# Kernel optimization log

Hardware: AMD Instinct MI355X
Metric: run time of the kernel (lower is better)

Reference implementation:

```python
import jax, jax.numpy as jnp
import numpy as np

B = 32768   # batch
F = 32      # per-node feature dim
H = 256     # hidden width
M = 4       # modules per node
OUT = 8     # final output dim
INIT_W = 0.003
B_INIT = 0.1


def _lin(k, din, dout):
    # fanin_init-style uniform weights, bias filled with 0.1 (hidden layers)
    s = 1.0 / np.sqrt(din)
    W = jax.random.uniform(k, (M, din, dout), jnp.float32, -s, s)
    b = jnp.full((M, dout), B_INIT, jnp.float32)
    return W, b


def setup_inputs() -> dict:
    key = jax.random.key(0)
    ks = jax.random.split(key, 16)
    feats = jax.random.normal(ks[0], (B, 4 * F), jnp.float32)
    idx = jax.random.randint(ks[1], (B, 4), 0, M)
    onehots = jax.nn.one_hot(idx, M, dtype=jnp.float32).reshape(B, 4 * M)
    input_val = jnp.concatenate([feats, onehots], axis=1)  # [B,144]

    W00, b00 = _lin(ks[2], F, H)        # node0 post layer 0
    W01, b01 = _lin(ks[3], H, H)        # node0 post layer 1
    Wpre1, bpre1 = _lin(ks[4], F, H)    # node1 pre
    Wpost1, bpost1 = _lin(ks[5], 2 * H, H)  # node1 interface (prev 256 + own 256)
    Wpre2, bpre2 = _lin(ks[6], F, H)
    Wpost2, bpost2 = _lin(ks[7], 2 * H, H)
    Wpre3, bpre3 = _lin(ks[8], F, H)
    Wpost3, bpost3 = _lin(ks[9], 2 * H, H)
    # final output layer: uniform(-init_w, init_w) for W and b, identity act
    Wfin3 = jax.random.uniform(ks[10], (M, H, OUT), jnp.float32, -INIT_W, INIT_W)
    bfin3 = jax.random.uniform(ks[11], (M, OUT), jnp.float32, -INIT_W, INIT_W)
    return dict(input_val=input_val,
                W00=W00, b00=b00, W01=W01, b01=b01,
                Wpre1=Wpre1, bpre1=bpre1, Wpost1=Wpost1, bpost1=bpost1,
                Wpre2=Wpre2, bpre2=bpre2, Wpost2=Wpost2, bpost2=bpost2,
                Wpre3=Wpre3, bpre3=bpre3, Wpost3=Wpost3, bpost3=bpost3,
                Wfin3=Wfin3, bfin3=bfin3)


def _select(h, onehot):
    # per-row pick of the assigned module's output: [B,M,D],[B,M] -> [B,D]
    return jnp.einsum('bmo,bm->bo', h, onehot)


def reference(input_val, W00, b00, W01, b01,
              Wpre1, bpre1, Wpost1, bpost1,
              Wpre2, bpre2, Wpost2, bpost2,
              Wpre3, bpre3, Wpost3, bpost3,
              Wfin3, bfin3):
    feat = lambda j: input_val[:, j * F:(j + 1) * F]
    oh = lambda j: input_val[:, 4 * F + j * M: 4 * F + (j + 1) * M]

    # node 0: two hidden layers, module-dispatched (dense-all-modules + one-hot combine)
    h = jax.nn.relu(jnp.einsum('bi,mio->bmo', feat(0), W00) + b00)
    h = jax.nn.relu(jnp.einsum('bmi,mio->bmo', h, W01) + b01)
    x = _select(h, oh(0))  # [B,H]

    def node(x_prev, fj, ohj, Wpre, bpre, Wpost, bpost):
        hp = jax.nn.relu(jnp.einsum('bi,mio->bmo', fj, Wpre) + bpre)
        # interface layer consumes concat([x_prev, hp]); split the weight to
        # avoid materializing [B,M,2H]
        hq = jax.nn.relu(jnp.einsum('bi,mio->bmo', x_prev, Wpost[:, :H, :])
                         + jnp.einsum('bmi,mio->bmo', hp, Wpost[:, H:, :])
                         + bpost)
        return hq  # [B,M,H]

    x = _select(node(x, feat(1), oh(1), Wpre1, bpre1, Wpost1, bpost1), oh(1))
    x = _select(node(x, feat(2), oh(2), Wpre2, bpre2, Wpost2, bpost2), oh(2))

    h3 = node(x, feat(3), oh(3), Wpre3, bpre3, Wpost3, bpost3)  # [B,M,H]
    out = jnp.einsum('bmi,mio->bmo', h3, Wfin3) + bfin3          # final linear, identity act
    return _select(out, oh(3))  # [B,OUT]
```

## Files before the change

kernel.cpp:

```cpp
#include <hip/hip_runtime.h>

#define NB 32768
#define MAXTILE 768

typedef short s8v __attribute__((ext_vector_type(8)));
typedef float f4v __attribute__((ext_vector_type(4)));
typedef unsigned short u16;
typedef unsigned int u32;
typedef unsigned char u8;

__device__ __forceinline__ float bf2f(u16 u) { return __uint_as_float(((u32)u) << 16); }
__device__ __forceinline__ u16 f2bf(float f) {
    u32 x = __float_as_uint(f);
    x += 0x7FFFu + ((x >> 16) & 1u);
    return (u16)(x >> 16);
}
__device__ __forceinline__ s8v ld8(const u16* p) { return *reinterpret_cast<const s8v*>(p); }

#define MFMA16(a, b, c) __builtin_amdgcn_mfma_f32_16x16x32_bf16((a), (b), (c), 0, 0, 0)

__global__ void probe_kernel(const void* __restrict__ input, int* __restrict__ flagp)
{
    int lane = threadIdx.x;
    u32 w = ((const u32*)input)[lane];
    u32 h0 = w & 0xFFFFu;
    u32 e0 = (h0 >> 7) & 0xFFu;
    bool plaus = (h0 == 0u) || (e0 >= 96u && e0 <= 143u);
    unsigned long long m = __ballot(plaus);
    if (lane == 0) *flagp = (__popcll(m) >= 48) ? 1 : 0;
}

struct Ent { const void* src; u16* dst; int Ksrc; int kBase; int S; };
struct RepackArgs { Ent d[11]; };
struct BEnt { const void* src; int dstOff; int n; };
struct BiasArgs { BEnt d[10]; };

__global__ __launch_bounds__(256) void prepA_kernel(const void* __restrict__ inputv,
                                                    const int* __restrict__ flagp,
                                                    int* __restrict__ counters,
                                                    u8* __restrict__ keys,
                                                    u16* __restrict__ inB,
                                                    u16* __restrict__ cbias,
                                                    RepackArgs A, BiasArgs BA)
{
    int flag = *flagp;
    if (blockIdx.x < 128) {
        __shared__ int lcnt[256];
        int tid = threadIdx.x;
        lcnt[tid] = 0;
        __syncthreads();
        int row = (blockIdx.x << 8) + tid;
        const u32* in32 = (const u32*)inputv;
        const u16* in16 = (const u16*)inputv;
        int key = 0;
#pragma unroll
        for (int j = 0; j < 4; j++) {
            int base = row * 144 + 128 + j * 4;
            u32 v1, v2, v3;
            if (flag) { v1 = in16[base + 1]; v2 = in16[base + 2]; v3 = in16[base + 3]; }
            else      { v1 = in32[base + 1]; v2 = in32[base + 2]; v3 = in32[base + 3]; }
            int m = v1 ? 1 : (v2 ? 2 : (v3 ? 3 : 0));
            key |= m << (j << 1);
        }
        keys[row] = (u8)key;
        atomicAdd(&lcnt[key], 1);
        __syncthreads();
        if (lcnt[tid]) atomicAdd(&counters[tid], lcnt[tid]);
    } else {
        const int RTOT = 131072 + 7 * 262144;
        const int BTOT = 8 * 1024 + 8192 + 32;
        const int PHA = RTOT + BTOT;
        int gtid = (blockIdx.x - 128) * 256 + threadIdx.x;
        int gstr = (gridDim.x - 128) * 256;
        int TOT = flag ? PHA : PHA + NB * 144;
        for (int i = gtid; i < TOT; i += gstr) {
            if (i < RTOT) {
                int e, local;
                if (i < 131072) { e = i >> 15; local = i & 32767; }
                else { int t = i - 131072; e = 4 + (t >> 18); local = t & 262143; }
                Ent d = A.d[e];
                int jj = local & 7, lane = (local >> 3) & 63, ct = (local >> 9) & 15;
                int m, s;
                if (d.S == 1) { m = local >> 13; s = 0; }
                else          { m = local >> 16; s = (local >> 13) & 7; }
                int k = d.kBase + s * 32 + ((lane >> 4) << 3) + jj;
                int n = (ct << 4) + (lane & 15);
                int idx = (m * d.Ksrc + k) * 256 + n;
                d.dst[local] = flag ? ((const u16*)d.src)[idx]
                                    : f2bf(((const float*)d.src)[idx]);
            } else if (i < PHA) {
                int t = i - RTOT;
                for (int e = 0; e < 10; e++) {
                    BEnt b = BA.d[e];
                    if (t < b.n) {
                        cbias[b.dstOff + t] = flag ? ((const u16*)b.src)[t]
                                                   : f2bf(((const float*)b.src)[t]);
                        break;
                    }
                    t -= b.n;
                }
            } else {
                int t = i - PHA;
                inB[t] = f2bf(((const float*)inputv)[t]);
            }
        }
    }
}

__global__ __launch_bounds__(256) void scan_kernel(const int* __restrict__ counters,
                                                   int* __restrict__ cursors,
                                                   int4* __restrict__ tileInfo)
{
    __shared__ int sbuf[256];
    __shared__ int tot;
    int tid = threadIdx.x;
    int c = counters[tid];
    sbuf[tid] = c;
    __syncthreads();
    for (int off = 1; off < 256; off <<= 1) {
        int v = (tid >= off) ? sbuf[tid - off] : 0;
        __syncthreads();
        sbuf[tid] += v;
        __syncthreads();
    }
    int base = sbuf[tid] - c;
    cursors[tid] = base;
    int tiles = (c + 63) >> 6;
    __syncthreads();
    sbuf[tid] = tiles;
    __syncthreads();
    for (int off = 1; off < 256; off <<= 1) {
        int v = (tid >= off) ? sbuf[tid - off] : 0;
        __syncthreads();
        sbuf[tid] += v;
        __syncthreads();
    }
    int tbase = sbuf[tid] - tiles;
    if (tid == 255) tot = sbuf[255];
    __syncthreads();
    for (int t = 0; t < tiles; t++) {
        int rem = c - t * 64;
        tileInfo[tbase + t] = make_int4(tid, base + t * 64, rem > 64 ? 64 : rem, 0);
    }
    for (int i = tot + tid; i < MAXTILE; i += 256)
        tileInfo[i] = make_int4(0, 0, 0, 0);
}

__global__ __launch_bounds__(256) void prepB_kernel(const u8* __restrict__ keys,
                                                    int* __restrict__ cursors,
                                                    int* __restrict__ perm)
{
    __shared__ int lcnt[256];
    __shared__ int lbase[256];
    int tid = threadIdx.x;
    lcnt[tid] = 0;
    __syncthreads();
    int row = (blockIdx.x << 8) + tid;
    int key = keys[row];
    int loc = atomicAdd(&lcnt[key], 1);
    __syncthreads();
    if (lcnt[tid]) lbase[tid] = atomicAdd(&cursors[tid], lcnt[tid]);
    __syncthreads();
    perm[lbase[key] + loc] = row;
}

struct MainW {
    const u16* pre[4];
    const u16* A[4];
    const u16* B[4];
    int bpre[4];
    int bmain[4];
};

__global__ __launch_bounds__(512, 4) void main_kernel(
    const void* __restrict__ inRaw, const u16* __restrict__ inB,
    const int* __restrict__ flagp,
    const int* __restrict__ perm, const int4* __restrict__ tileInfo,
    const u16* __restrict__ cbias, MainW W, void* __restrict__ outp)
{
    __shared__ __align__(16) u16 xc[64 * 264];
    __shared__ __align__(16) u16 hp[64 * 264];
    __shared__ __align__(16) u16 wfl[8 * 264];
    __shared__ int rowids[64];

    int tid = threadIdx.x;
    int lane = tid & 63, wave = tid >> 6, quad = lane >> 4, l16 = lane & 15;

    int4 ti = tileInfo[blockIdx.x];
    int key = ti.x, ppos = ti.y, cntIn = ti.z;
    if (cntIn <= 0) return;
    int flag = *flagp;
    const u16* ip = flag ? (const u16*)inRaw : inB;

    if (tid < 64) {
        int g = tid < cntIn ? tid : cntIn - 1;
        rowids[tid] = perm[ppos + g];
    }
    {
        int m3 = (key >> 6) & 3;
        const u16* Wf = cbias + 8192;
        for (int i = tid; i < 2048; i += 512) {
            int k = i & 255, o = i >> 8;
            wfl[o * 264 + k] = Wf[(((m3 << 8) + k) << 3) + o];
        }
    }
    __syncthreads();

    int ct0 = wave << 1;

    for (int node = 0; node < 4; node++) {
        int m = (key >> (node << 1)) & 3;

        {
            const s8v* Bp = (const s8v*)W.pre[node] + (m << 4) * 64 + lane;
            const u16* bb = cbias + W.bpre[node] + (m << 8);
#pragma unroll
            for (int rt = 0; rt < 4; rt++) {
                int row = rowids[(rt << 4) + l16];
                s8v a = ld8(ip + row * 144 + (node << 5) + (quad << 3));
#pragma unroll
                for (int ci = 0; ci < 2; ci++) {
                    int ct = ct0 + ci;
                    f4v c = {0.f, 0.f, 0.f, 0.f};
                    c = MFMA16(a, Bp[ct * 64], c);
                    float bv = bf2f(bb[(ct << 4) + l16]);
#pragma unroll
                    for (int r = 0; r < 4; r++) {
                        float v = c[r] + bv; v = v > 0.f ? v : 0.f;
                        hp[((rt << 4) + (quad << 2) + r) * 264 + (ct << 4) + l16] = f2bf(v);
                    }
                }
            }
        }
        __syncthreads();

        f4v acc[4][2];
#pragma unroll
        for (int i = 0; i < 4; i++) { acc[i][0] = (f4v){0,0,0,0}; acc[i][1] = (f4v){0,0,0,0}; }

        if (node > 0) {
            const s8v* BA = (const s8v*)W.A[node];
#pragma unroll
            for (int s = 0; s < 8; s++) {
                s8v a0 = ld8(&xc[(l16) * 264 + (s << 5) + (quad << 3)]);
                s8v a1 = ld8(&xc[(16 + l16) * 264 + (s << 5) + (quad << 3)]);
                s8v a2 = ld8(&xc[(32 + l16) * 264 + (s << 5) + (quad << 3)]);
                s8v a3 = ld8(&xc[(48 + l16) * 264 + (s << 5) + (quad << 3)]);
#pragma unroll
                for (int ci = 0; ci < 2; ci++) {
                    s8v bv = BA[((((m << 3) + s) << 4) + ct0 + ci) * 64 + lane];
                    acc[0][ci] = MFMA16(a0, bv, acc[0][ci]);
                    acc[1][ci] = MFMA16(a1, bv, acc[1][ci]);
                    acc[2][ci] = MFMA16(a2, bv, acc[2][ci]);
                    acc[3][ci] = MFMA16(a3, bv, acc[3][ci]);
                }
            }
        }
        {
            const s8v* BB = (const s8v*)W.B[node];
#pragma unroll
            for (int s = 0; s < 8; s++) {
                s8v a0 = ld8(&hp[(l16) * 264 + (s << 5) + (quad << 3)]);
                s8v a1 = ld8(&hp[(16 + l16) * 264 + (s << 5) + (quad << 3)]);
                s8v a2 = ld8(&hp[(32 + l16) * 264 + (s << 5) + (quad << 3)]);
                s8v a3 = ld8(&hp[(48 + l16) * 264 + (s << 5) + (quad << 3)]);
#pragma unroll
                for (int ci = 0; ci < 2; ci++) {
                    s8v bv = BB[((((m << 3) + s) << 4) + ct0 + ci) * 64 + lane];
                    acc[0][ci] = MFMA16(a0, bv, acc[0][ci]);
                    acc[1][ci] = MFMA16(a1, bv, acc[1][ci]);
                    acc[2][ci] = MFMA16(a2, bv, acc[2][ci]);
                    acc[3][ci] = MFMA16(a3, bv, acc[3][ci]);
                }
            }
        }
        __syncthreads();

        {
            const u16* bm = cbias + W.bmain[node] + (m << 8);
#pragma unroll
            for (int ci = 0; ci < 2; ci++) {
                int colb = ((ct0 + ci) << 4) + l16;
                float bv = bf2f(bm[colb]);
#pragma unroll
                for (int rt = 0; rt < 4; rt++) {
#pragma unroll
                    for (int r = 0; r < 4; r++) {
                        float v = acc[rt][ci][r] + bv; v = v > 0.f ? v : 0.f;
                        xc[((rt << 4) + (quad << 2) + r) * 264 + colb] = f2bf(v);
                    }
                }
            }
        }
        __syncthreads();
    }

    {
        int m3 = (key >> 6) & 3;
        int r = tid >> 3, o = tid & 7;
        float s = bf2f(cbias[16384 + (m3 << 3) + o]);
        const u16* hrow = &xc[r * 264];
        const u16* wrow = &wfl[o * 264];
        for (int k = 0; k < 256; k += 8) {
            s8v h8 = ld8(hrow + k);
            s8v w8 = ld8(wrow + k);
#pragma unroll
            for (int j = 0; j < 8; j++) s += bf2f((u16)h8[j]) * bf2f((u16)w8[j]);
        }
        if (r < cntIn) {
            int oi = (rowids[r] << 3) + o;
            if (flag) ((u16*)outp)[oi] = f2bf(s);
            else      ((float*)outp)[oi] = s;
        }
    }
}

extern "C" void kernel_launch(void* const* d_in, const int* in_sizes, int n_in,
                              void* d_out, int out_size, void* d_ws, size_t ws_size,
                              hipStream_t stream)
{
    (void)in_sizes; (void)n_in; (void)out_size;
    const void* input  = d_in[0];
    const void* W00    = d_in[1];
    const void* b00    = d_in[2];
    const void* W01    = d_in[3];
    const void* b01    = d_in[4];
    const void* Wpre1  = d_in[5];
    const void* bpre1  = d_in[6];
    const void* Wpost1 = d_in[7];
    const void* bpost1 = d_in[8];
    const void* Wpre2  = d_in[9];
    const void* bpre2  = d_in[10];
    const void* Wpost2 = d_in[11];
    const void* bpost2 = d_in[12];
    const void* Wpre3  = d_in[13];
    const void* bpre3  = d_in[14];
    const void* Wpost3 = d_in[15];
    const void* bpost3 = d_in[16];
    const void* Wfin   = d_in[17];
    const void* bfin   = d_in[18];

    char* base = (char*)d_ws;
    size_t off = 0;
    auto alloc = [&](size_t bytes) -> char* {
        char* p = base + off;
        off += (bytes + 255) & ~(size_t)255;
        return p;
    };
    int*  flagp    = (int*)alloc(4);
    int*  counters = (int*)alloc(256 * 4);
    int*  cursors  = (int*)alloc(256 * 4);
    u8*   keys     = (u8*)alloc(NB);
    int4* tileInfo = (int4*)alloc(MAXTILE * 16);
    int*  perm     = (int*)alloc((size_t)NB * 4);
    u16*  cbias    = (u16*)alloc(16640 * 2);
    u16*  inB      = (u16*)alloc((size_t)NB * 144 * 2);
    u16* rW00   = (u16*)alloc(32768 * 2);
    u16* rWpre1 = (u16*)alloc(32768 * 2);
    u16* rWpre2 = (u16*)alloc(32768 * 2);
    u16* rWpre3 = (u16*)alloc(32768 * 2);
    u16* rW01 = (u16*)alloc(262144 * 2);
    u16* rW1A = (u16*)alloc(262144 * 2);
    u16* rW1B = (u16*)alloc(262144 * 2);
    u16* rW2A = (u16*)alloc(262144 * 2);
    u16* rW2B = (u16*)alloc(262144 * 2);
    u16* rW3A = (u16*)alloc(262144 * 2);
    u16* rW3B = (u16*)alloc(262144 * 2);
    if (off > ws_size) return;

    hipMemsetAsync(counters, 0, 256 * 4, stream);
    probe_kernel<<<1, 64, 0, stream>>>(input, flagp);

    RepackArgs ra;
    ra.d[0]  = Ent{W00,    rW00,   32,   0, 1};
    ra.d[1]  = Ent{Wpre1,  rWpre1, 32,   0, 1};
    ra.d[2]  = Ent{Wpre2,  rWpre2, 32,   0, 1};
    ra.d[3]  = Ent{Wpre3,  rWpre3, 32,   0, 1};
    ra.d[4]  = Ent{W01,    rW01,  256,   0, 8};
    ra.d[5]  = Ent{Wpost1, rW1A,  512,   0, 8};
    ra.d[6]  = Ent{Wpost1, rW1B,  512, 256, 8};
    ra.d[7]  = Ent{Wpost2, rW2A,  512,   0, 8};
    ra.d[8]  = Ent{Wpost2, rW2B,  512, 256, 8};
    ra.d[9]  = Ent{Wpost3, rW3A,  512,   0, 8};
    ra.d[10] = Ent{Wpost3, rW3B,  512, 256, 8};

    BiasArgs ba;
    ba.d[0] = BEnt{b00,    0,     1024};
    ba.d[1] = BEnt{b01,    1024,  1024};
    ba.d[2] = BEnt{bpre1,  2048,  1024};
    ba.d[3] = BEnt{bpost1, 3072,  1024};
    ba.d[4] = BEnt{bpre2,  4096,  1024};
    ba.d[5] = BEnt{bpost2, 5120,  1024};
    ba.d[6] = BEnt{bpre3,  6144,  1024};
    ba.d[7] = BEnt{bpost3, 7168,  1024};
    ba.d[8] = BEnt{Wfin,   8192,  8192};
    ba.d[9] = BEnt{bfin,   16384, 32};

    prepA_kernel<<<128 + 1536, 256, 0, stream>>>(input, flagp, counters, keys, inB, cbias, ra, ba);
    scan_kernel<<<1, 256, 0, stream>>>(counters, cursors, tileInfo);
    prepB_kernel<<<128, 256, 0, stream>>>(keys, cursors, perm);

    MainW W;
    W.pre[0] = rW00;   W.pre[1] = rWpre1; W.pre[2] = rWpre2; W.pre[3] = rWpre3;
    W.A[0]   = nullptr; W.A[1]  = rW1A;   W.A[2]   = rW2A;   W.A[3]   = rW3A;
    W.B[0]   = rW01;   W.B[1]   = rW1B;   W.B[2]   = rW2B;   W.B[3]   = rW3B;
    W.bpre[0] = 0;    W.bpre[1] = 2048; W.bpre[2] = 4096; W.bpre[3] = 6144;
    W.bmain[0] = 1024; W.bmain[1] = 3072; W.bmain[2] = 5120; W.bmain[3] = 7168;

    main_kernel<<<MAXTILE, 512, 0, stream>>>(input, inB, flagp, perm, tileInfo, cbias, W, d_out);
}
```

Measured before the change: 203.7 us.

## Restructure main kernel with transposed MFMA, fused concat buffer, and tiled weight repack

The main kernel now computes the transposed product (weights as the A operand, activations as B) and keeps the previous node output and the pre-layer output side by side in one LDS buffer. The interface layer therefore runs as a single K=512 loop, with a register prefetch of the next weight slice and bias folded into the accumulator init. The full-input bf16 conversion pass is dropped: fp32 inputs are converted on the fly inside the main kernel. Weight repacking moves to a separate kernel that transposes through LDS per tile, the final layer uses MFMA instead of a scalar dot product, and the counter memset is folded into the probe kernel. The goal is less preprocessing traffic and fewer launches, at the cost of more complex indexing and larger LDS rows.

```diff
diff --git a/kernel.cpp b/kernel.cpp
--- a/kernel.cpp
+++ b/kernel.cpp
@@ -2,10 +2,13 @@
 
 #define NB 32768
 #define MAXTILE 768
+#define XHS 536
 
 typedef short s8v __attribute__((ext_vector_type(8)));
+typedef short s4v __attribute__((ext_vector_type(4)));
 typedef float f4v __attribute__((ext_vector_type(4)));
 typedef unsigned short u16;
+typedef unsigned short u16x4 __attribute__((ext_vector_type(4)));
 typedef unsigned int u32;
 typedef unsigned char u8;
 
@@ -19,92 +22,49 @@
 
 #define MFMA16(a, b, c) __builtin_amdgcn_mfma_f32_16x16x32_bf16((a), (b), (c), 0, 0, 0)
 
-__global__ void probe_kernel(const void* __restrict__ input, int* __restrict__ flagp)
-{
-    int lane = threadIdx.x;
-    u32 w = ((const u32*)input)[lane];
-    u32 h0 = w & 0xFFFFu;
-    u32 e0 = (h0 >> 7) & 0xFFu;
-    bool plaus = (h0 == 0u) || (e0 >= 96u && e0 <= 143u);
-    unsigned long long m = __ballot(plaus);
-    if (lane == 0) *flagp = (__popcll(m) >= 48) ? 1 : 0;
-}
-
-struct Ent { const void* src; u16* dst; int Ksrc; int kBase; int S; };
-struct RepackArgs { Ent d[11]; };
-struct BEnt { const void* src; int dstOff; int n; };
-struct BiasArgs { BEnt d[10]; };
+__global__ __launch_bounds__(256) void probe_kernel(const void* __restrict__ input,
+                                                    int* __restrict__ flagp,
+                                                    int* __restrict__ counters)
+{
+    int tid = threadIdx.x;
+    counters[tid] = 0;
+    if (tid < 64) {
+        u32 w = ((const u32*)input)[tid];
+        u32 h0 = w & 0xFFFFu;
+        u32 e0 = (h0 >> 7) & 0xFFu;
+        bool plaus = (h0 == 0u) || (e0 >= 96u && e0 <= 143u);
+        unsigned long long m = __ballot(plaus);
+        if (tid == 0) *flagp = (__popcll(m) >= 48) ? 1 : 0;
+    }
+}
 
 __global__ __launch_bounds__(256) void prepA_kernel(const void* __restrict__ inputv,
                                                     const int* __restrict__ flagp,
                                                     int* __restrict__ counters,
-                                                    u8* __restrict__ keys,
-                                                    u16* __restrict__ inB,
-                                                    u16* __restrict__ cbias,
-                                                    RepackArgs A, BiasArgs BA)
-{
+                                                    u8* __restrict__ keys)
+{
+    __shared__ int lcnt[256];
     int flag = *flagp;
-    if (blockIdx.x < 128) {
-        __shared__ int lcnt[256];
-        int tid = threadIdx.x;
-        lcnt[tid] = 0;
-        __syncthreads();
-        int row = (blockIdx.x << 8) + tid;
-        const u32* in32 = (const u32*)inputv;
-        const u16* in16 = (const u16*)inputv;
-        int key = 0;
-#pragma unroll
-        for (int j = 0; j < 4; j++) {
-            int base = row * 144 + 128 + j * 4;
-            u32 v1, v2, v3;
-            if (flag) { v1 = in16[base + 1]; v2 = in16[base + 2]; v3 = in16[base + 3]; }
-            else      { v1 = in32[base + 1]; v2 = in32[base + 2]; v3 = in32[base + 3]; }
-            int m = v1 ? 1 : (v2 ? 2 : (v3 ? 3 : 0));
-            key |= m << (j << 1);
-        }
-        keys[row] = (u8)key;
-        atomicAdd(&lcnt[key], 1);
-        __syncthreads();
-        if (lcnt[tid]) atomicAdd(&counters[tid], lcnt[tid]);
-    } else {
-        const int RTOT = 131072 + 7 * 262144;
-        const int BTOT = 8 * 1024 + 8192 + 32;
-        const int PHA = RTOT + BTOT;
-        int gtid = (blockIdx.x - 128) * 256 + threadIdx.x;
-        int gstr = (gridDim.x - 128) * 256;
-        int TOT = flag ? PHA : PHA + NB * 144;
-        for (int i = gtid; i < TOT; i += gstr) {
-            if (i < RTOT) {
-                int e, local;
-                if (i < 131072) { e = i >> 15; local = i & 32767; }
-                else { int t = i - 131072; e = 4 + (t >> 18); local = t & 262143; }
-                Ent d = A.d[e];
-                int jj = local & 7, lane = (local >> 3) & 63, ct = (local >> 9) & 15;
-                int m, s;
-                if (d.S == 1) { m = local >> 13; s = 0; }
-                else          { m = local >> 16; s = (local >> 13) & 7; }
-                int k = d.kBase + s * 32 + ((lane >> 4) << 3) + jj;
-                int n = (ct << 4) + (lane & 15);
-                int idx = (m * d.Ksrc + k) * 256 + n;
-                d.dst[local] = flag ? ((const u16*)d.src)[idx]
-                                    : f2bf(((const float*)d.src)[idx]);
-            } else if (i < PHA) {
-                int t = i - RTOT;
-                for (int e = 0; e < 10; e++) {
-                    BEnt b = BA.d[e];
-                    if (t < b.n) {
-                        cbias[b.dstOff + t] = flag ? ((const u16*)b.src)[t]
-                                                   : f2bf(((const float*)b.src)[t]);
-                        break;
-                    }
-                    t -= b.n;
-                }
-            } else {
-                int t = i - PHA;
-                inB[t] = f2bf(((const float*)inputv)[t]);
-            }
-        }
-    }
+    int tid = threadIdx.x;
+    lcnt[tid] = 0;
+    __syncthreads();
+    int row = (blockIdx.x << 8) + tid;
+    const u32* in32 = (const u32*)inputv;
+    const u16* in16 = (const u16*)inputv;
+    int key = 0;
+#pragma unroll
+    for (int j = 0; j < 4; j++) {
+        int base = row * 144 + 128 + j * 4;
+        u32 v1, v2, v3;
+        if (flag) { v1 = in16[base + 1]; v2 = in16[base + 2]; v3 = in16[base + 3]; }
+        else      { v1 = in32[base + 1]; v2 = in32[base + 2]; v3 = in32[base + 3]; }
+        int m = v1 ? 1 : (v2 ? 2 : (v3 ? 3 : 0));
+        key |= m << (j << 1);
+    }
+    keys[row] = (u8)key;
+    atomicAdd(&lcnt[key], 1);
+    __syncthreads();
+    if (lcnt[tid]) atomicAdd(&counters[tid], lcnt[tid]);
 }
 
 __global__ __launch_bounds__(256) void scan_kernel(const int* __restrict__ counters,
@@ -164,153 +124,217 @@
     perm[lbase[key] + loc] = row;
 }
 
-struct MainW {
-    const u16* pre[4];
-    const u16* A[4];
-    const u16* B[4];
-    int bpre[4];
-    int bmain[4];
+struct RepArgs {
+    const void* W01; const void* Wp[3]; const void* pre[4]; const void* fin;
+    const void* bias[9];
+    u16 *rPre, *rW01, *rWp[3], *rFin, *cbias;
 };
 
+__global__ __launch_bounds__(256) void repack_kernel(const int* __restrict__ flagp, RepArgs R)
+{
+    __shared__ u16 T[8192];
+    int flag = *flagp;
+    int tid = threadIdx.x;
+    int b = blockIdx.x;
+
+    const void* src = nullptr; u16* dst = nullptr; int K = 0, k0 = 0, mrow = 0;
+    if (b < 32) {
+        int m = b >> 3, s = b & 7;
+        src = R.W01; dst = R.rW01 + (m * 8 + s) * 8192; K = 256; k0 = s * 32; mrow = m;
+    } else if (b < 224) {
+        int idx = b - 32, mat = idx >> 6, r = idx & 63, m = r >> 4, s = r & 15;
+        src = R.Wp[mat]; dst = R.rWp[mat] + (m * 16 + s) * 8192; K = 512; k0 = s * 32; mrow = m;
+    } else if (b < 240) {
+        int idx = b - 224, mat = idx >> 2, m = idx & 3;
+        src = R.pre[mat]; dst = R.rPre + (mat * 4 + m) * 8192; K = 32; k0 = 0; mrow = m;
+    } else if (b < 244) {
+        int m = b - 240;
+        const u16* s16 = (const u16*)R.fin;
+        const float* s32 = (const float*)R.fin;
+        for (int i = tid; i < 2048; i += 256) {
+            int si = (m * 256 + (i >> 3)) * 8 + (i & 7);
+            T[i] = flag ? s16[si] : f2bf(s32[si]);
+        }
+        __syncthreads();
+        u16* d = R.rFin + m * 4096;
+        for (int i = tid; i < 4096; i += 256) {
+            int s = i >> 9, lane = (i >> 3) & 63, j = i & 7;
+            int q = lane >> 4, l16 = lane & 15;
+            int k = s * 32 + q * 8 + j;
+            d[i] = (l16 < 8) ? T[k * 8 + l16] : (u16)0;
+        }
+        return;
+    } else {
+        const int sz[9] = {1024,1024,1024,1024,1024,1024,1024,1024,32};
+        const int of[9] = {0,1024,2048,3072,4096,5120,6144,7168,8192};
+        for (int i = tid; i < 8224; i += 256) {
+            int t = i, e = 0;
+            while (t >= sz[e]) { t -= sz[e]; e++; }
+            R.cbias[of[e] + t] = flag ? ((const u16*)R.bias[e])[t]
+                                      : f2bf(((const float*)R.bias[e])[t]);
+        }
+        return;
+    }
+
+    const u16* s16 = (const u16*)src;
+    const float* s32 = (const float*)src;
+    for (int i = tid; i < 8192; i += 256) {
+        int k = i >> 8, n = i & 255;
+        int srcIdx = (mrow * K + k0 + k) * 256 + n;
+        T[i] = flag ? s16[srcIdx] : f2bf(s32[srcIdx]);
+    }
+    __syncthreads();
+    for (int i = tid; i < 8192; i += 256) {
+        int mt = i >> 9, lane = (i >> 3) & 63, j = i & 7;
+        int k = ((lane >> 4) << 3) + j, n = (mt << 4) + (lane & 15);
+        dst[i] = T[(k << 8) + n];
+    }
+}
+
+struct MainP { const u16 *rPre, *rW01, *rWp1, *rWp2, *rWp3, *rFin, *cbias; };
+
 __global__ __launch_bounds__(512, 4) void main_kernel(
-    const void* __restrict__ inRaw, const u16* __restrict__ inB,
-    const int* __restrict__ flagp,
+    const void* __restrict__ inRaw, const int* __restrict__ flagp,
     const int* __restrict__ perm, const int4* __restrict__ tileInfo,
-    const u16* __restrict__ cbias, MainW W, void* __restrict__ outp)
-{
-    __shared__ __align__(16) u16 xc[64 * 264];
-    __shared__ __align__(16) u16 hp[64 * 264];
-    __shared__ __align__(16) u16 wfl[8 * 264];
+    MainP P, void* __restrict__ outp)
+{
+    __shared__ __align__(16) u16 xh[64 * XHS];
     __shared__ int rowids[64];
 
     int tid = threadIdx.x;
-    int lane = tid & 63, wave = tid >> 6, quad = lane >> 4, l16 = lane & 15;
+    int lane = tid & 63, w = tid >> 6, quad = lane >> 4, l16 = lane & 15;
 
     int4 ti = tileInfo[blockIdx.x];
     int key = ti.x, ppos = ti.y, cntIn = ti.z;
     if (cntIn <= 0) return;
     int flag = *flagp;
-    const u16* ip = flag ? (const u16*)inRaw : inB;
 
     if (tid < 64) {
         int g = tid < cntIn ? tid : cntIn - 1;
         rowids[tid] = perm[ppos + g];
     }
-    {
-        int m3 = (key >> 6) & 3;
-        const u16* Wf = cbias + 8192;
-        for (int i = tid; i < 2048; i += 512) {
-            int k = i & 255, o = i >> 8;
-            wfl[o * 264 + k] = Wf[(((m3 << 8) + k) << 3) + o];
-        }
-    }
-    __syncthreads();
-
-    int ct0 = wave << 1;
+    __syncthreads();
+    int rows[4];
+#pragma unroll
+    for (int nt = 0; nt < 4; nt++) rows[nt] = rowids[nt * 16 + l16];
+
+    const u16* mainW[4] = {P.rW01, P.rWp1, P.rWp2, P.rWp3};
+    const u16* in16 = (const u16*)inRaw;
+    const float* in32 = (const float*)inRaw;
 
     for (int node = 0; node < 4; node++) {
         int m = (key >> (node << 1)) & 3;
 
+        s8v fb[4];
+#pragma unroll
+        for (int nt = 0; nt < 4; nt++) {
+            int off = rows[nt] * 144 + (node << 5) + (quad << 3);
+            if (flag) fb[nt] = ld8(in16 + off);
+            else {
+                f4v f0 = *(const f4v*)(in32 + off);
+                f4v f1 = *(const f4v*)(in32 + off + 4);
+                s8v r;
+#pragma unroll
+                for (int j = 0; j < 4; j++) { r[j] = (short)f2bf(f0[j]); r[4 + j] = (short)f2bf(f1[j]); }
+                fb[nt] = r;
+            }
+        }
+
+        const u16* preB = P.rPre + ((node << 2) + m) * 8192;
+#pragma unroll
+        for (int ci = 0; ci < 2; ci++) {
+            int mt = (w << 1) + ci;
+            s8v a = ld8(preB + mt * 512 + lane * 8);
+            u16x4 bv = *(const u16x4*)(P.cbias + node * 2048 + m * 256 + mt * 16 + quad * 4);
+            f4v bias;
+#pragma unroll
+            for (int r = 0; r < 4; r++) bias[r] = bf2f(bv[r]);
+#pragma unroll
+            for (int nt = 0; nt < 4; nt++) {
+                f4v c = MFMA16(a, fb[nt], bias);
+                s4v p;
+#pragma unroll
+                for (int r = 0; r < 4; r++) { float v = c[r] > 0.f ? c[r] : 0.f; p[r] = (short)f2bf(v); }
+                *(s4v*)&xh[(nt * 16 + l16) * XHS + 256 + mt * 16 + quad * 4] = p;
+            }
+        }
+        __syncthreads();
+
+        int s0 = node ? 0 : 8;
+        const u16* WB = mainW[node] + m * (node ? 16 : 8) * 8192;
+        f4v acc[2][4];
         {
-            const s8v* Bp = (const s8v*)W.pre[node] + (m << 4) * 64 + lane;
-            const u16* bb = cbias + W.bpre[node] + (m << 8);
-#pragma unroll
-            for (int rt = 0; rt < 4; rt++) {
-                int row = rowids[(rt << 4) + l16];
-                s8v a = ld8(ip + row * 144 + (node << 5) + (quad << 3));
-#pragma unroll
-                for (int ci = 0; ci < 2; ci++) {
-                    int ct = ct0 + ci;
-                    f4v c = {0.f, 0.f, 0.f, 0.f};
-                    c = MFMA16(a, Bp[ct * 64], c);
-                    float bv = bf2f(bb[(ct << 4) + l16]);
-#pragma unroll
-                    for (int r = 0; r < 4; r++) {
-                        float v = c[r] + bv; v = v > 0.f ? v : 0.f;
-                        hp[((rt << 4) + (quad << 2) + r) * 264 + (ct << 4) + l16] = f2bf(v);
-                    }
+            u16x4 b0 = *(const u16x4*)(P.cbias + node * 2048 + 1024 + m * 256 + ((w << 1) + 0) * 16 + quad * 4);
+            u16x4 b1 = *(const u16x4*)(P.cbias + node * 2048 + 1024 + m * 256 + ((w << 1) + 1) * 16 + quad * 4);
+            f4v f0, f1;
+#pragma unroll
+            for (int r = 0; r < 4; r++) { f0[r] = bf2f(b0[r]); f1[r] = bf2f(b1[r]); }
+#pragma unroll
+            for (int nt = 0; nt < 4; nt++) { acc[0][nt] = f0; acc[1][nt] = f1; }
+        }
+        {
+            s8v A0 = ld8(WB + (w << 1) * 512 + lane * 8);
+            s8v A1 = ld8(WB + ((w << 1) + 1) * 512 + lane * 8);
+#pragma unroll
+            for (int s = s0; s < 16; s++) {
+                s8v nA0 = A0, nA1 = A1;
+                if (s + 1 < 16) {
+                    const u16* nb = WB + (s + 1 - s0) * 8192;
+                    nA0 = ld8(nb + (w << 1) * 512 + lane * 8);
+                    nA1 = ld8(nb + ((w << 1) + 1) * 512 + lane * 8);
                 }
+#pragma unroll
+                for (int nt = 0; nt < 4; nt++) {
+                    s8v B = ld8(&xh[(nt * 16 + l16) * XHS + s * 32 + quad * 8]);
+                    acc[0][nt] = MFMA16(A0, B, acc[0][nt]);
+                    acc[1][nt] = MFMA16(A1, B, acc[1][nt]);
+                }
+                A0 = nA0;
+                A1 = nA1;
             }
         }
         __syncthreads();
 
-        f4v acc[4][2];
-#pragma unroll
-        for (int i = 0; i < 4; i++) { acc[i][0] = (f4v){0,0,0,0}; acc[i][1] = (f4v){0,0,0,0}; }
-
-        if (node > 0) {
-            const s8v* BA = (const s8v*)W.A[node];
-#pragma unroll
-            for (int s = 0; s < 8; s++) {
-                s8v a0 = ld8(&xc[(l16) * 264 + (s << 5) + (quad << 3)]);
-                s8v a1 = ld8(&xc[(16 + l16) * 264 + (s << 5) + (quad << 3)]);
-                s8v a2 = ld8(&xc[(32 + l16) * 264 + (s << 5) + (quad << 3)]);
-                s8v a3 = ld8(&xc[(48 + l16) * 264 + (s << 5) + (quad << 3)]);
-#pragma unroll
-                for (int ci = 0; ci < 2; ci++) {
-                    s8v bv = BA[((((m << 3) + s) << 4) + ct0 + ci) * 64 + lane];
-                    acc[0][ci] = MFMA16(a0, bv, acc[0][ci]);
-                    acc[1][ci] = MFMA16(a1, bv, acc[1][ci]);
-                    acc[2][ci] = MFMA16(a2, bv, acc[2][ci]);
-                    acc[3][ci] = MFMA16(a3, bv, acc[3][ci]);
+#pragma unroll
+        for (int ci = 0; ci < 2; ci++) {
+            int mt = (w << 1) + ci;
+#pragma unroll
+            for (int nt = 0; nt < 4; nt++) {
+                s4v p;
+#pragma unroll
+                for (int r = 0; r < 4; r++) {
+                    float v = acc[ci][nt][r]; v = v > 0.f ? v : 0.f;
+                    p[r] = (short)f2bf(v);
                 }
+                *(s4v*)&xh[(nt * 16 + l16) * XHS + mt * 16 + quad * 4] = p;
             }
         }
-        {
-            const s8v* BB = (const s8v*)W.B[node];
-#pragma unroll
-            for (int s = 0; s < 8; s++) {
-                s8v a0 = ld8(&hp[(l16) * 264 + (s << 5) + (quad << 3)]);
-                s8v a1 = ld8(&hp[(16 + l16) * 264 + (s << 5) + (quad << 3)]);
-                s8v a2 = ld8(&hp[(32 + l16) * 264 + (s << 5) + (quad << 3)]);
-                s8v a3 = ld8(&hp[(48 + l16) * 264 + (s << 5) + (quad << 3)]);
-#pragma unroll
-                for (int ci = 0; ci < 2; ci++) {
-                    s8v bv = BB[((((m << 3) + s) << 4) + ct0 + ci) * 64 + lane];
-                    acc[0][ci] = MFMA16(a0, bv, acc[0][ci]);
-                    acc[1][ci] = MFMA16(a1, bv, acc[1][ci]);
-                    acc[2][ci] = MFMA16(a2, bv, acc[2][ci]);
-                    acc[3][ci] = MFMA16(a3, bv, acc[3][ci]);
-                }
+    }
+    __syncthreads();
+
+    if (w < 4) {
+        int m3 = (key >> 6) & 3;
+        f4v c;
+#pragma unroll
+        for (int r = 0; r < 4; r++)
+            c[r] = (quad < 2) ? bf2f(P.cbias[8192 + m3 * 8 + quad * 4 + r]) : 0.f;
+#pragma unroll
+        for (int s = 0; s < 8; s++) {
+            s8v A = ld8(P.rFin + m3 * 4096 + s * 512 + lane * 8);
+            s8v B = ld8(&xh[(w * 16 + l16) * XHS + s * 32 + quad * 8]);
+            c = MFMA16(A, B, c);
+        }
+        int bidx = w * 16 + l16;
+        if (quad < 2 && bidx < cntIn) {
+            int row = rowids[bidx];
+            if (flag) {
+                s4v p;
+#pragma unroll
+                for (int r = 0; r < 4; r++) p[r] = (short)f2bf(c[r]);
+                *(s4v*)((u16*)outp + row * 8 + quad * 4) = p;
+            } else {
+                *(f4v*)((float*)outp + row * 8 + quad * 4) = c;
             }
-        }
-        __syncthreads();
-
-        {
-            const u16* bm = cbias + W.bmain[node] + (m << 8);
-#pragma unroll
-            for (int ci = 0; ci < 2; ci++) {
-                int colb = ((ct0 + ci) << 4) + l16;
-                float bv = bf2f(bm[colb]);
-#pragma unroll
-                for (int rt = 0; rt < 4; rt++) {
-#pragma unroll
-                    for (int r = 0; r < 4; r++) {
-                        float v = acc[rt][ci][r] + bv; v = v > 0.f ? v : 0.f;
-                        xc[((rt << 4) + (quad << 2) + r) * 264 + colb] = f2bf(v);
-                    }
-                }
-            }
-        }
-        __syncthreads();
-    }
-
-    {
-        int m3 = (key >> 6) & 3;
-        int r = tid >> 3, o = tid & 7;
-        float s = bf2f(cbias[16384 + (m3 << 3) + o]);
-        const u16* hrow = &xc[r * 264];
-        const u16* wrow = &wfl[o * 264];
-        for (int k = 0; k < 256; k += 8) {
-            s8v h8 = ld8(hrow + k);
-            s8v w8 = ld8(wrow + k);
-#pragma unroll
-            for (int j = 0; j < 8; j++) s += bf2f((u16)h8[j]) * bf2f((u16)w8[j]);
-        }
-        if (r < cntIn) {
-            int oi = (rowids[r] << 3) + o;
-            if (flag) ((u16*)outp)[oi] = f2bf(s);
-            else      ((float*)outp)[oi] = s;
         }
     }
 }
@@ -353,59 +377,36 @@
     u8*   keys     = (u8*)alloc(NB);
     int4* tileInfo = (int4*)alloc(MAXTILE * 16);
     int*  perm     = (int*)alloc((size_t)NB * 4);
-    u16*  cbias    = (u16*)alloc(16640 * 2);
-    u16*  inB      = (u16*)alloc((size_t)NB * 144 * 2);
-    u16* rW00   = (u16*)alloc(32768 * 2);
-    u16* rWpre1 = (u16*)alloc(32768 * 2);
-    u16* rWpre2 = (u16*)alloc(32768 * 2);
-    u16* rWpre3 = (u16*)alloc(32768 * 2);
-    u16* rW01 = (u16*)alloc(262144 * 2);
-    u16* rW1A = (u16*)alloc(262144 * 2);
-    u16* rW1B = (u16*)alloc(262144 * 2);
-    u16* rW2A = (u16*)alloc(262144 * 2);
-    u16* rW2B = (u16*)alloc(262144 * 2);
-    u16* rW3A = (u16*)alloc(262144 * 2);
-    u16* rW3B = (u16*)alloc(262144 * 2);
+    u16*  cbias    = (u16*)alloc(8224 * 2);
+    u16*  rPre     = (u16*)alloc(131072 * 2);
+    u16*  rW01     = (u16*)alloc(262144 * 2);
+    u16*  rWp1     = (u16*)alloc(524288 * 2);
+    u16*  rWp2     = (u16*)alloc(524288 * 2);
+    u16*  rWp3     = (u16*)alloc(524288 * 2);
+    u16*  rFin     = (u16*)alloc(16384 * 2);
     if (off > ws_size) return;
 
-    hipMemsetAsync(counters, 0, 256 * 4, stream);
-    probe_kernel<<<1, 64, 0, stream>>>(input, flagp);
-
-    RepackArgs ra;
-    ra.d[0]  = Ent{W00,    rW00,   32,   0, 1};
-    ra.d[1]  = Ent{Wpre1,  rWpre1, 32,   0, 1};
-    ra.d[2]  = Ent{Wpre2,  rWpre2, 32,   0, 1};
-    ra.d[3]  = Ent{Wpre3,  rWpre3, 32,   0, 1};
-    ra.d[4]  = Ent{W01,    rW01,  256,   0, 8};
-    ra.d[5]  = Ent{Wpost1, rW1A,  512,   0, 8};
-    ra.d[6]  = Ent{Wpost1, rW1B,  512, 256, 8};
-    ra.d[7]  = Ent{Wpost2, rW2A,  512,   0, 8};
-    ra.d[8]  = Ent{Wpost2, rW2B,  512, 256, 8};
-    ra.d[9]  = Ent{Wpost3, rW3A,  512,   0, 8};
-    ra.d[10] = Ent{Wpost3, rW3B,  512, 256, 8};
-
-    BiasArgs ba;
-    ba.d[0] = BEnt{b00,    0,     1024};
-    ba.d[1] = BEnt{b01,    1024,  1024};
-    ba.d[2] = BEnt{bpre1,  2048,  1024};
-    ba.d[3] = BEnt{bpost1, 3072,  1024};
-    ba.d[4] = BEnt{bpre2,  4096,  1024};
-    ba.d[5] = BEnt{bpost2, 5120,  1024};
-    ba.d[6] = BEnt{bpre3,  6144,  1024};
-    ba.d[7] = BEnt{bpost3, 7168,  1024};
-    ba.d[8] = BEnt{Wfin,   8192,  8192};
-    ba.d[9] = BEnt{bfin,   16384, 32};
-
-    prepA_kernel<<<128 + 1536, 256, 0, stream>>>(input, flagp, counters, keys, inB, cbias, ra, ba);
+    probe_kernel<<<1, 256, 0, stream>>>(input, flagp, counters);
+    prepA_kernel<<<128, 256, 0, stream>>>(input, flagp, counters, keys);
     scan_kernel<<<1, 256, 0, stream>>>(counters, cursors, tileInfo);
     prepB_kernel<<<128, 256, 0, stream>>>(keys, cursors, perm);
 
-    MainW W;
-    W.pre[0] = rW00;   W.pre[1] = rWpre1; W.pre[2] = rWpre2; W.pre[3] = rWpre3;
-    W.A[0]   = nullptr; W.A[1]  = rW1A;   W.A[2]   = rW2A;   W.A[3]   = rW3A;
-    W.B[0]   = rW01;   W.B[1]   = rW1B;   W.B[2]   = rW2B;   W.B[3]   = rW3B;
-    W.bpre[0] = 0;    W.bpre[1] = 2048; W.bpre[2] = 4096; W.bpre[3] = 6144;
-    W.bmain[0] = 1024; W.bmain[1] = 3072; W.bmain[2] = 5120; W.bmain[3] = 7168;
-
-    main_kernel<<<MAXTILE, 512, 0, stream>>>(input, inB, flagp, perm, tileInfo, cbias, W, d_out);
-}
+    RepArgs R;
+    R.W01 = W01; R.Wp[0] = Wpost1; R.Wp[1] = Wpost2; R.Wp[2] = Wpost3;
+    R.pre[0] = W00; R.pre[1] = Wpre1; R.pre[2] = Wpre2; R.pre[3] = Wpre3;
+    R.fin = Wfin;
+    R.bias[0] = b00;   R.bias[1] = b01;
+    R.bias[2] = bpre1; R.bias[3] = bpost1;
+    R.bias[4] = bpre2; R.bias[5] = bpost2;
+    R.bias[6] = bpre3; R.bias[7] = bpost3;
+    R.bias[8] = bfin;
+    R.rPre = rPre; R.rW01 = rW01;
+    R.rWp[0] = rWp1; R.rWp[1] = rWp2; R.rWp[2] = rWp3;
+    R.rFin = rFin; R.cbias = cbias;
+    repack_kernel<<<245, 256, 0, stream>>>(flagp, R);
+
+    MainP P;
+    P.rPre = rPre; P.rW01 = rW01; P.rWp1 = rWp1; P.rWp2 = rWp2; P.rWp3 = rWp3;
+    P.rFin = rFin; P.cbias = cbias;
+    main_kernel<<<MAXTILE, 512, 0, stream>>>(input, flagp, perm, tileInfo, P, d_out);
+}
```

Result: no change. 200.3 us (-1.7%).
